# Performance work log

Measured on AMD Instinct MI355X. Metric: run time of the kernel, lower is better.

## Reference

```python
import jax, jax.numpy as jnp
import numpy as np

NEG_SLOPE = 0.2
LN_EPS = 1e-5


def _layer_norm(x, w, b):
    mu = jnp.mean(x, axis=-1, keepdims=True)
    var = jnp.mean((x - mu) ** 2, axis=-1, keepdims=True)
    return (x - mu) / jnp.sqrt(var + LN_EPS) * w + b


def setup_inputs() -> dict:
    N, E, R, H, D, HID, FF = 50000, 800000, 8, 4, 32, 128, 512
    key = jax.random.key(0)
    ks = jax.random.split(key, 12)
    s_w = float(np.sqrt(2.0 / (HID + HID)))  # xavier-ish scale
    return {
        "x": jax.random.normal(ks[0], (N, HID), jnp.float32),
        "weight": jax.random.normal(ks[1], (R, HID, HID), jnp.float32) * s_w,
        "root_weight": jax.random.normal(ks[2], (HID, HID), jnp.float32) * s_w,
        "edge_emb_table": jax.random.normal(ks[3], (R, HID), jnp.float32) * 0.01,
        "att_src": jax.random.normal(ks[4], (1, H, D), jnp.float32) * 0.1,
        "att_dst": jax.random.normal(ks[5], (1, H, D), jnp.float32) * 0.1,
        "att_edge": jax.random.normal(ks[6], (1, H, D), jnp.float32) * 0.1,
        "bias": jnp.zeros((HID,), jnp.float32),
        "norm1_w": jnp.ones((HID,), jnp.float32),
        "norm1_b": jnp.zeros((HID,), jnp.float32),
        "norm2_w": jnp.ones((HID,), jnp.float32),
        "norm2_b": jnp.zeros((HID,), jnp.float32),
        "ffn_w1": jax.random.normal(ks[7], (HID, FF), jnp.float32) * float(np.sqrt(2.0 / (HID + FF))),
        "ffn_b1": jnp.zeros((FF,), jnp.float32),
        "ffn_w2": jax.random.normal(ks[8], (FF, HID), jnp.float32) * float(np.sqrt(2.0 / (HID + FF))),
        "ffn_b2": jnp.zeros((HID,), jnp.float32),
        "edge_index": jax.random.randint(ks[9], (2, E), 0, N, jnp.int32),
        "edge_type": jax.random.randint(ks[10], (E,), 0, R, jnp.int32),
    }


def _rgat_conv(h, edge_index, edge_type, weight, root_weight, edge_emb_table,
               att_src, att_dst, att_edge, bias):
    N = h.shape[0]
    R = weight.shape[0]
    H, D = att_src.shape[1], att_src.shape[2]
    # relation-wise projection: [R, N, H, D]
    x_r = jnp.einsum('ni,rio->rno', h, weight).reshape(R, N, H, D)
    src, dst = edge_index[0], edge_index[1]
    x_src = x_r[edge_type, src]            # [E, H, D]
    x_dst = x_r[edge_type, dst]            # [E, H, D]
    edge_emb = edge_emb_table[edge_type].reshape(-1, H, D)
    alpha = (x_src * att_src).sum(-1) + (x_dst * att_dst).sum(-1) + (edge_emb * att_edge).sum(-1)  # [E, H]
    alpha = jax.nn.leaky_relu(alpha, NEG_SLOPE)
    # segment softmax over destination nodes
    amax = jax.ops.segment_max(alpha, dst, num_segments=N)  # [N, H]
    amax = jnp.where(jnp.isfinite(amax), amax, 0.0)
    ex = jnp.exp(alpha - amax[dst])
    den = jax.ops.segment_sum(ex, dst, num_segments=N)
    alpha = ex / (den[dst] + 1e-16)
    # dropout is identity in eval mode
    msg = x_src * alpha[..., None]         # [E, H, D]
    out = jax.ops.segment_sum(msg, dst, num_segments=N).reshape(N, H * D)
    return out + h @ root_weight + bias


def reference(x, weight, root_weight, edge_emb_table, att_src, att_dst, att_edge,
              bias, norm1_w, norm1_b, norm2_w, norm2_b,
              ffn_w1, ffn_b1, ffn_w2, ffn_b2, edge_index, edge_type):
    h = _layer_norm(x, norm1_w, norm1_b)
    h = _rgat_conv(h, edge_index, edge_type, weight, root_weight, edge_emb_table,
                   att_src, att_dst, att_edge, bias)
    h = jax.nn.elu(h)
    x = x + h
    h = _layer_norm(x, norm2_w, norm2_b)
    h = jax.nn.gelu(h @ ffn_w1 + ffn_b1, approximate=False) @ ffn_w2 + ffn_b2
    return x + h
```

## Files before the change

kernel.cpp:

```cpp
#include <hip/hip_runtime.h>
#include <hip/hip_bf16.h>
#include <math.h>

#define HID 128
#define NH  4
#define HD  32
#define FFD 512
#define RR  8
#define SCAN_B 1024
#define NB_SH 6

typedef __attribute__((ext_vector_type(8))) short bf16x8;
typedef __attribute__((ext_vector_type(4))) float f32x4;
typedef unsigned short u16;
typedef unsigned long long u64;

static __device__ __forceinline__ float bf2f(u16 u) {
    union { unsigned int i; float f; } v; v.i = ((unsigned int)u) << 16; return v.f;
}
static __device__ __forceinline__ u16 f2bf(float f) {
    union { float f; unsigned int i; } v; v.f = f;
    unsigned int x = v.i;
    return (u16)((x + 0x7fffu + ((x >> 16) & 1u)) >> 16);
}

__global__ void zeroout_kernel(float* out, int n) {
    int i = blockIdx.x * 256 + threadIdx.x;
    if (i < n) out[i] = 0.f;
}

__global__ void init_kernel(float* acc, int* deg2, int* bcnt, int NN, int NBK) {
    int i = blockIdx.x * 256 + threadIdx.x;
    if (i < NN * HID) acc[i] = 0.f;
    if (i < NN * RR) deg2[i] = 0;
    if (i < NBK * 16) bcnt[i] = 0;
}

__global__ void stats_kernel(const float* in, float* mu, float* rs, int NN) {
    int row = blockIdx.x * 4 + (threadIdx.x >> 6);
    int lane = threadIdx.x & 63;
    if (row >= NN) return;
    const float* p = in + (size_t)row * HID;
    float v0 = p[lane], v1 = p[lane + 64];
    float s = v0 + v1;
    #pragma unroll
    for (int o = 32; o > 0; o >>= 1) s += __shfl_xor(s, o, 64);
    float m = s * (1.0f / HID);
    float d0 = v0 - m, d1 = v1 - m;
    float q = d0 * d0 + d1 * d1;
    #pragma unroll
    for (int o = 32; o > 0; o >>= 1) q += __shfl_xor(q, o, 64);
    if (lane == 0) { mu[row] = m; rs[row] = rsqrtf(q * (1.0f / HID) + 1e-5f); }
}

__global__ void hnorm_kernel(const float* in, const float* mu, const float* rs,
                             const float* lw, const float* lb, u16* out, int NN) {
    int idx = blockIdx.x * 256 + threadIdx.x;
    if (idx >= NN * (HID / 8)) return;
    int row = idx >> 4;
    int k0 = (idx & 15) * 8;
    float m = mu[row], r = rs[row];
    const float* p = in + (size_t)row * HID + k0;
    float4 a0 = *(const float4*)p, a1 = *(const float4*)(p + 4);
    float4 w0 = *(const float4*)(lw + k0), w1 = *(const float4*)(lw + k0 + 4);
    float4 b0 = *(const float4*)(lb + k0), b1 = *(const float4*)(lb + k0 + 4);
    bf16x8 o;
    o[0] = (short)f2bf((a0.x - m) * r * w0.x + b0.x);
    o[1] = (short)f2bf((a0.y - m) * r * w0.y + b0.y);
    o[2] = (short)f2bf((a0.z - m) * r * w0.z + b0.z);
    o[3] = (short)f2bf((a0.w - m) * r * w0.w + b0.w);
    o[4] = (short)f2bf((a1.x - m) * r * w1.x + b1.x);
    o[5] = (short)f2bf((a1.y - m) * r * w1.y + b1.y);
    o[6] = (short)f2bf((a1.z - m) * r * w1.z + b1.z);
    o[7] = (short)f2bf((a1.w - m) * r * w1.w + b1.w);
    *(bf16x8*)(out + (size_t)row * HID + k0) = o;
}

__global__ void transpose_kernel(const float* w, const float* rootw,
                                 const float* w1, const float* w2,
                                 u16* WT, u16* rootT, u16* W1T, u16* W2T, int R) {
    int i = blockIdx.x * 256 + threadIdx.x;
    int nW = R * HID * HID;
    if (i < nW) {
        int r = i / (HID * HID); int rem = i % (HID * HID);
        int n = rem / HID, k = rem % HID;
        WT[i] = f2bf(w[r * HID * HID + k * HID + n]);
    } else if (i < nW + HID * HID) {
        int j = i - nW; int n = j / HID, k = j % HID;
        rootT[j] = f2bf(rootw[k * HID + n]);
    } else if (i < nW + HID * HID + FFD * HID) {
        int j = i - nW - HID * HID; int n = j / HID, k = j % HID;
        W1T[j] = f2bf(w1[k * FFD + n]);
    } else if (i < nW + HID * HID + FFD * HID + HID * FFD) {
        int j = i - nW - HID * HID - FFD * HID; int n = j / FFD, k = j % FFD;
        W2T[j] = f2bf(w2[k * HID + n]);
    }
}

__global__ void vsd_kernel(const float* w, const float* att_src, const float* att_dst,
                           u16* Vsd, int R) {
    int idx = blockIdx.x * 256 + threadIdx.x;
    if (idx >= 64 * HID) return;
    int np = idx >> 7, k = idx & 127;
    int isDst = np >> 5, rh = np & 31, r = rh >> 2, h = rh & 3;
    const float* av = (isDst ? att_dst : att_src) + h * HD;
    const float* wp = w + (size_t)r * HID * HID + (size_t)k * HID + h * HD;
    float s = 0.f;
    #pragma unroll
    for (int d = 0; d < HD; d++) s += wp[d] * av[d];
    Vsd[idx] = f2bf(s);
}

__global__ void ae_kernel(const float* emb, const float* att_edge, float* ae, int R) {
    int i = threadIdx.x;
    if (i >= R * NH) return;
    int r = i >> 2, h = i & 3;
    float s = 0.f;
    #pragma unroll
    for (int d = 0; d < HD; d++)
        s += emb[r * HID + h * HD + d] * att_edge[h * HD + d];
    ae[i] = s;
}

template <int EPI>
__global__ __launch_bounds__(256)
void gemmy_kernel(const u16* Araw, const u16* BT, u16* Cout, const float* bias,
                  int M, int N, int aOff, int cOff, int ytiles) {
    int w = threadIdx.x >> 6, lane = threadIdx.x & 63;
    int l15 = lane & 15, quad = lane >> 4;
    int m0 = blockIdx.x * 64 + w * 16;
    int rowA = m0 + l15; if (rowA > M - 1) rowA = M - 1;
    const u16* ap = Araw + (size_t)(aOff + rowA) * HID + quad * 8;
    bf16x8 a[4];
    #pragma unroll
    for (int kk = 0; kk < 4; kk++) a[kk] = *(const bf16x8*)(ap + kk * 32);

    __shared__ u16 tile[64][72];
    int rl2 = threadIdx.x >> 3, seg = threadIdx.x & 7;
    int ybase = blockIdx.y * ytiles;
    for (int yi = 0; yi < ytiles; yi++) {
        int n0 = (ybase + yi) * 64;
        f32x4 accr[4] = {};
        #pragma unroll
        for (int kk = 0; kk < 4; kk++) {
            #pragma unroll
            for (int t = 0; t < 4; t++) {
                const u16* bp = BT + (size_t)(n0 + t * 16 + l15) * HID + quad * 8 + kk * 32;
                bf16x8 bfrag = *(const bf16x8*)bp;
                accr[t] = __builtin_amdgcn_mfma_f32_16x16x32_bf16(a[kk], bfrag, accr[t], 0, 0, 0);
            }
        }
        if (yi > 0) __syncthreads();
        #pragma unroll
        for (int t = 0; t < 4; t++) {
            int col = n0 + t * 16 + l15;
            #pragma unroll
            for (int j = 0; j < 4; j++) {
                float v = accr[t][j];
                if constexpr (EPI == 2) {
                    v += bias[col];
                    v = 0.5f * v * (1.0f + erff(v * 0.70710678118654752f));
                }
                tile[w * 16 + quad * 4 + j][t * 16 + l15] = f2bf(v);
            }
        }
        __syncthreads();
        #pragma unroll
        for (int h = 0; h < 2; h++) {
            int rl = h * 32 + rl2;
            int row = blockIdx.x * 64 + rl;
            if (row < M) {
                u16* dst = Cout + (size_t)(cOff + row) * N + n0 + seg * 8;
                __builtin_nontemporal_store(*(const bf16x8*)&tile[rl][seg * 8],
                                            (bf16x8*)dst);
            }
        }
    }
}

template <int AM, int EPI>
__global__ __launch_bounds__(256)
void gemm_kernel(const void* Araw, const float* mu, const float* rs,
                 const float* lw, const float* lb,
                 const u16* BT, void* Cout, const float* bias,
                 const float* acc, const float* xin, const float* invden,
                 int M, int N, int K, int aOff, int cOff) {
    int w = threadIdx.x >> 6, lane = threadIdx.x & 63;
    int l15 = lane & 15, quad = lane >> 4;
    int m0 = blockIdx.x * 64 + w * 16;
    int n0 = blockIdx.y * 64;
    int rowA = m0 + l15; if (rowA > M - 1) rowA = M - 1;
    int gA = aOff + rowA;
    float muv = 0.f, rsv = 0.f;
    if (AM != 2) { muv = mu[gA]; rsv = rs[gA]; }

    f32x4 accr[4] = {};
    for (int kc = 0; kc < K; kc += 32) {
        bf16x8 a;
        if (AM == 0) {
            const float* ap = (const float*)Araw + (size_t)gA * K + quad * 8 + kc;
            float4 xa0 = *(const float4*)(ap);
            float4 xa1 = *(const float4*)(ap + 4);
            float4 w0 = *(const float4*)(lw + kc + quad * 8);
            float4 w1v = *(const float4*)(lw + kc + quad * 8 + 4);
            float4 b0 = *(const float4*)(lb + kc + quad * 8);
            float4 b1v = *(const float4*)(lb + kc + quad * 8 + 4);
            a[0] = (short)f2bf((xa0.x - muv) * rsv * w0.x + b0.x);
            a[1] = (short)f2bf((xa0.y - muv) * rsv * w0.y + b0.y);
            a[2] = (short)f2bf((xa0.z - muv) * rsv * w0.z + b0.z);
            a[3] = (short)f2bf((xa0.w - muv) * rsv * w0.w + b0.w);
            a[4] = (short)f2bf((xa1.x - muv) * rsv * w1v.x + b1v.x);
            a[5] = (short)f2bf((xa1.y - muv) * rsv * w1v.y + b1v.y);
            a[6] = (short)f2bf((xa1.z - muv) * rsv * w1v.z + b1v.z);
            a[7] = (short)f2bf((xa1.w - muv) * rsv * w1v.w + b1v.w);
        } else {
            const u16* ap = (const u16*)Araw + (size_t)gA * K + quad * 8 + kc;
            a = *(const bf16x8*)ap;
        }
        #pragma unroll
        for (int t = 0; t < 4; t++) {
            const u16* bp = BT + (size_t)(n0 + t * 16 + l15) * K + quad * 8 + kc;
            bf16x8 bfrag = *(const bf16x8*)bp;
            accr[t] = __builtin_amdgcn_mfma_f32_16x16x32_bf16(a, bfrag, accr[t], 0, 0, 0);
        }
    }

    if constexpr (EPI == 0 || EPI == 2) {
        __shared__ u16 tile[64][72];
        #pragma unroll
        for (int t = 0; t < 4; t++) {
            int col = n0 + t * 16 + l15;
            #pragma unroll
            for (int j = 0; j < 4; j++) {
                float v = accr[t][j];
                if (EPI == 2) {
                    v += bias[col];
                    v = 0.5f * v * (1.0f + erff(v * 0.70710678118654752f));
                }
                tile[w * 16 + quad * 4 + j][t * 16 + l15] = f2bf(v);
            }
        }
        __syncthreads();
        int rl2 = threadIdx.x >> 3, seg = threadIdx.x & 7;
        #pragma unroll
        for (int h = 0; h < 2; h++) {
            int rl = h * 32 + rl2;
            int row = blockIdx.x * 64 + rl;
            if (row < M) {
                u16* dst = (u16*)Cout + (size_t)(cOff + row) * N + n0 + seg * 8;
                __builtin_nontemporal_store(*(const bf16x8*)&tile[rl][seg * 8],
                                            (bf16x8*)dst);
            }
        }
    } else {
        #pragma unroll
        for (int t = 0; t < 4; t++) {
            int col = n0 + t * 16 + l15;
            #pragma unroll
            for (int j = 0; j < 4; j++) {
                int row = m0 + quad * 4 + j;
                if (row < M) {
                    float v = accr[t][j];
                    int grow = cOff + row;
                    size_t off = (size_t)grow * N + col;
                    if (EPI == 1) {
                        float msg = acc[(size_t)grow * HID + col]
                                  * invden[(size_t)grow * NH + (col >> 5)];
                        float o = v + msg + bias[col];
                        o = o > 0.f ? o : expm1f(o);
                        ((float*)Cout)[off] = xin[off] + o;
                    } else if (EPI == 3) {
                        ((float*)Cout)[off] = v + bias[col] + xin[off];
                    } else if (EPI == 5) {
                        float* tab = (float*)Cout;
                        if (col < 32) tab[(size_t)grow * 32 + col] = v;
                        else tab[(size_t)(M + grow) * 32 + (col - 32)] = v;
                    }
                }
            }
        }
    }
}

__global__ void deg_kernel(const int* ei, const int* et, int* deg2, int E, int NN) {
    int e = blockIdx.x * 256 + threadIdx.x;
    if (e >= E) return;
    int s = ei[e], d = ei[E + e], r = et[e];
    if ((unsigned)d < (unsigned)NN && (unsigned)r < (unsigned)RR &&
        (unsigned)s < (unsigned)NN)
        atomicAdd(&deg2[d * RR + r], 1);
}

__global__ void scan1_kernel(const int* in, int* out, int* bsum, int n) {
    __shared__ int buf[SCAN_B];
    int i = blockIdx.x * SCAN_B + threadIdx.x;
    int v = (i < n) ? in[i] : 0;
    buf[threadIdx.x] = v;
    __syncthreads();
    for (int s = 1; s < SCAN_B; s <<= 1) {
        int t = (threadIdx.x >= s) ? buf[threadIdx.x - s] : 0;
        __syncthreads();
        buf[threadIdx.x] += t;
        __syncthreads();
    }
    if (i < n) out[i] = buf[threadIdx.x] - v;
    if (threadIdx.x == SCAN_B - 1) bsum[blockIdx.x] = buf[SCAN_B - 1];
}

__global__ void scan2_kernel(int* bsum, int nb) {
    __shared__ int buf[SCAN_B];
    int v = (threadIdx.x < nb) ? bsum[threadIdx.x] : 0;
    buf[threadIdx.x] = v;
    __syncthreads();
    for (int s = 1; s < SCAN_B; s <<= 1) {
        int t = (threadIdx.x >= s) ? buf[threadIdx.x - s] : 0;
        __syncthreads();
        buf[threadIdx.x] += t;
        __syncthreads();
    }
    if (threadIdx.x < nb) bsum[threadIdx.x] = buf[threadIdx.x] - v;
    if (threadIdx.x == SCAN_B - 1) bsum[nb] = buf[SCAN_B - 1];
}

__global__ void scan3_kernel(int* out, int* curpos, const int* bsum, int n, int nb) {
    int i = blockIdx.x * SCAN_B + threadIdx.x;
    if (i < n) {
        int o = out[i] + bsum[blockIdx.x];
        out[i] = o; curpos[i] = o;
    }
    if (i == 0) out[n] = bsum[nb];
}

__global__ void fillA_kernel(const int* ei, const int* et, const int* offs2,
                             int* bcnt, u64* tmp, int E, int NN) {
    int e = blockIdx.x * 256 + threadIdx.x;
    if (e >= E) return;
    int s = ei[e], d = ei[E + e], r = et[e];
    if ((unsigned)d >= (unsigned)NN || (unsigned)r >= (unsigned)RR ||
        (unsigned)s >= (unsigned)NN) return;
    int b = d >> NB_SH;
    int base = offs2[(b << NB_SH) * RR];
    int pos = atomicAdd(&bcnt[b * 16], 1);
    tmp[base + pos] = ((u64)d << 32) | (unsigned)((r << 24) | s);
}

__global__ void fillB_kernel(const u64* tmp, const int* offs2,
                             int* curpos2, int* rs_arr, int NN) {
    int b = blockIdx.x;
    int n0 = b << NB_SH;
    int n1 = n0 + (1 << NB_SH); if (n1 > NN) n1 = NN;
    int base = offs2[n0 * RR];
    int end  = offs2[n1 * RR];
    for (int i = base + threadIdx.x; i < end; i += 256) {
        u64 t = tmp[i];
        int d = (int)(t >> 32);
        unsigned v = (unsigned)t;
        int r = v >> 24;
        int pos = atomicAdd(&curpos2[d * RR + r], 1);
        rs_arr[pos] = (int)v;
    }
}

__global__ void wgt_kernel(const int* offs2, const int* rs_arr,
                           const float* asad, const float* ae,
                           float* wgt, float* invden, int NN, int E) {
    int n = blockIdx.x * 4 + (threadIdx.x >> 6);
    if (n >= NN) return;
    int lane = threadIdx.x & 63;
    int el = lane >> 2, h = lane & 3;
    int p0 = offs2[n * RR], p1 = offs2[n * RR + RR];
    const float* ad = asad + (size_t)NN * 32;
    float base[RR];
    #pragma unroll
    for (int r = 0; r < RR; r++)
        base[r] = ad[(size_t)n * 32 + r * 4 + h] + ae[r * 4 + h];
    float mx = -1e30f;
    for (int p = p0 + el; p < p1; p += 16) {
        unsigned v = (unsigned)rs_arr[p];
        int r = v >> 24, s = v & 0xFFFFFF;
        float a = asad[(size_t)s * 32 + r * 4 + h] + base[r];
        a = a > 0.f ? a : 0.2f * a;
        wgt[(size_t)p * NH + h] = a;
        mx = fmaxf(mx, a);
    }
    #pragma unroll
    for (int o = 4; o < 64; o <<= 1) mx = fmaxf(mx, __shfl_xor(mx, o, 64));
    float den = 0.f;
    for (int p = p0 + el; p < p1; p += 16) {
        float ex = __expf(wgt[(size_t)p * NH + h] - mx);
        wgt[(size_t)p * NH + h] = ex;
        den += ex;
    }
    #pragma unroll
    for (int o = 4; o < 64; o <<= 1) den += __shfl_xor(den, o, 64);
    if (el == 0) invden[n * NH + h] = 1.0f / (den + 1e-16f);
}

__global__ void msg2_kernel(const int* offs2, const int* rs_arr, const float* wgt,
                            const u16* xp, float* acc, int rc, int nrel, int ldx,
                            int NN, int E, int single) {
    int n = blockIdx.x;
    int c = threadIdx.x, h = c >> 5;
    int p0 = offs2[n * RR + rc], p1 = offs2[n * RR + rc + nrel];
    float av;
    if (single) {
        av = 0.f;
    } else {
        if (p0 >= p1) return;
        av = acc[(size_t)n * HID + c];
    }
    for (int p = p0; p < p1; p++) {
        unsigned v = (unsigned)rs_arr[p];
        int r = (v >> 24) - rc;
        int s = v & 0xFFFFFF;
        av += wgt[(size_t)p * NH + h] * bf2f(xp[(size_t)s * ldx + r * HID + c]);
    }
    acc[(size_t)n * HID + c] = av;
}

extern "C" void kernel_launch(void* const* d_in, const int* in_sizes, int n_in,
                              void* d_out, int out_size, void* d_ws, size_t ws_size,
                              hipStream_t stream) {
    const float* x        = (const float*)d_in[0];
    const float* w        = (const float*)d_in[1];
    const float* rootw    = (const float*)d_in[2];
    const float* emb      = (const float*)d_in[3];
    const float* att_src  = (const float*)d_in[4];
    const float* att_dst  = (const float*)d_in[5];
    const float* att_edge = (const float*)d_in[6];
    const float* bias     = (const float*)d_in[7];
    const float* n1w      = (const float*)d_in[8];
    const float* n1b      = (const float*)d_in[9];
    const float* n2w      = (const float*)d_in[10];
    const float* n2b      = (const float*)d_in[11];
    const float* w1       = (const float*)d_in[12];
    const float* b1       = (const float*)d_in[13];
    const float* w2       = (const float*)d_in[14];
    const float* b2       = (const float*)d_in[15];
    const int* ei = (const int*)d_in[16];
    const int* et = (const int*)d_in[17];

    int NN = in_sizes[0] / HID;
    int R  = in_sizes[1] / (HID * HID);
    int E  = in_sizes[17];
    int NR = NN * RR;
    int NBK = (NN + (1 << NB_SH) - 1) >> NB_SH;

    char* p = (char*)d_ws;
    auto alloc = [&](size_t bytes) -> char* {
        char* q = p; p += (bytes + 255) & ~(size_t)255; return q;
    };
    int* offs2   = (int*)alloc((size_t)(NR + 1) * 4);
    int* rs_arr  = (int*)alloc((size_t)E * 4);
    u16* WTw   = (u16*)alloc((size_t)R * HID * HID * 2);
    u16* rootT = (u16*)alloc((size_t)HID * HID * 2);
    u16* W1T   = (u16*)alloc((size_t)FFD * HID * 2);
    u16* W2T   = (u16*)alloc((size_t)HID * FFD * 2);
    u16* Vsd   = (u16*)alloc((size_t)64 * HID * 2);
    float* ae  = (float*)alloc((size_t)R * NH * 4);
    float* mu1 = (float*)alloc((size_t)NN * 4);
    float* rs1 = (float*)alloc((size_t)NN * 4);
    float* mu2 = (float*)alloc((size_t)NN * 4);
    float* rs2 = (float*)alloc((size_t)NN * 4);
    float* asad   = (float*)alloc((size_t)NN * 64 * 4);
    float* invden = (float*)alloc((size_t)NN * NH * 4);
    float* wgt    = (float*)alloc((size_t)E * NH * 4);
    float* acc    = (float*)alloc((size_t)NN * HID * 4);

    int nbScan = (NR + SCAN_B - 1) / SCAN_B;
    int* deg2    = (int*)wgt;
    int* curpos2 = deg2 + NR;
    int* bsum    = curpos2 + NR;
    int* bcnt    = bsum + nbScan + 1;
    u64* tmp     = (u64*)(((size_t)(bcnt + NBK * 16) + 7) & ~(size_t)7);

    size_t usedFixed = (size_t)(p - (char*)d_ws);
    int nrel = 1;
    for (int t = 8; t > 1; t >>= 1) {
        if (ws_size >= usedFixed + (size_t)NN * HID * t * 2 + 256) { nrel = t; break; }
    }
    u16* xp = (u16*)alloc((size_t)NN * HID * nrel * 2);
    u16* u_ch = xp;
    u16* hbuf = (u16*)asad;
    float* x2 = (float*)d_out;

    size_t used = (size_t)(p - (char*)d_ws);
    if (used > ws_size) {
        zeroout_kernel<<<(out_size + 255) / 256, 256, 0, stream>>>((float*)d_out, out_size);
        return;
    }

    init_kernel<<<(NN * HID + 255) / 256, 256, 0, stream>>>(acc, deg2, bcnt, NN, NBK);
    stats_kernel<<<(NN + 3) / 4, 256, 0, stream>>>(x, mu1, rs1, NN);
    int nT = R * HID * HID + HID * HID + FFD * HID + HID * FFD;
    transpose_kernel<<<(nT + 255) / 256, 256, 0, stream>>>(w, rootw, w1, w2,
                                                           WTw, rootT, W1T, W2T, R);
    vsd_kernel<<<(64 * HID + 255) / 256, 256, 0, stream>>>(w, att_src, att_dst, Vsd, R);
    ae_kernel<<<1, 64, 0, stream>>>(emb, att_edge, ae, R);
    deg_kernel<<<(E + 255) / 256, 256, 0, stream>>>(ei, et, deg2, E, NN);
    scan1_kernel<<<nbScan, SCAN_B, 0, stream>>>(deg2, offs2, bsum, NR);
    scan2_kernel<<<1, SCAN_B, 0, stream>>>(bsum, nbScan);
    scan3_kernel<<<nbScan, SCAN_B, 0, stream>>>(offs2, curpos2, bsum, NR, nbScan);
    fillA_kernel<<<(E + 255) / 256, 256, 0, stream>>>(ei, et, offs2, bcnt, tmp, E, NN);
    fillB_kernel<<<NBK, 256, 0, stream>>>(tmp, offs2, curpos2, rs_arr, NN);

    int gxN = (NN + 63) / 64;
    gemm_kernel<0, 5><<<dim3(gxN, 1), 256, 0, stream>>>(
        x, mu1, rs1, n1w, n1b, Vsd, asad,
        nullptr, nullptr, nullptr, nullptr, NN, 64, HID, 0, 0);

    wgt_kernel<<<(NN + 3) / 4, 256, 0, stream>>>(
        offs2, rs_arr, asad, ae, wgt, invden, NN, E);

    hnorm_kernel<<<(NN * (HID / 8) + 255) / 256, 256, 0, stream>>>(
        x, mu1, rs1, n1w, n1b, hbuf, NN);

    if (nrel == RR) {
        gemmy_kernel<0><<<dim3(gxN, 2), 256, 0, stream>>>(
            hbuf, WTw, xp, nullptr, NN, HID * RR, 0, 0, 8);
        msg2_kernel<<<NN, HID, 0, stream>>>(offs2, rs_arr, wgt, xp, acc,
                                            0, RR, HID * RR, NN, E, 1);
    } else {
        for (int rc = 0; rc < RR; rc += nrel) {
            gemm_kernel<2, 0><<<dim3(gxN, (HID * nrel) / 64), 256, 0, stream>>>(
                hbuf, nullptr, nullptr, nullptr, nullptr, WTw + (size_t)rc * HID * HID,
                xp, nullptr, nullptr, nullptr, nullptr, NN, HID * nrel, HID, 0, 0);
            msg2_kernel<<<NN, HID, 0, stream>>>(offs2, rs_arr, wgt, xp, acc,
                                                rc, nrel, HID * nrel, NN, E, 0);
        }
    }

    gemm_kernel<2, 1><<<dim3(gxN, HID / 64), 256, 0, stream>>>(
        hbuf, nullptr, nullptr, nullptr, nullptr, rootT, x2, bias, acc, x, invden,
        NN, HID, HID, 0, 0);

    stats_kernel<<<(NN + 3) / 4, 256, 0, stream>>>(x2, mu2, rs2, NN);
    hnorm_kernel<<<(NN * (HID / 8) + 255) / 256, 256, 0, stream>>>(
        x2, mu2, rs2, n2w, n2b, hbuf, NN);
    int nchunk = (nrel >= 4) ? 1 : (nrel == 2 ? 2 : 4);
    int NCH = (NN + nchunk - 1) / nchunk;
    for (int j = 0; j < nchunk; j++) {
        int r0 = j * NCH;
        int Mc = NN - r0; if (Mc > NCH) Mc = NCH;
        if (Mc <= 0) continue;
        int gxc = (Mc + 63) / 64;
        gemmy_kernel<2><<<dim3(gxc, 2), 256, 0, stream>>>(
            hbuf, W1T, u_ch, b1, Mc, FFD, r0, 0, 4);
        gemm_kernel<2, 3><<<dim3(gxc, HID / 64), 256, 0, stream>>>(
            u_ch, nullptr, nullptr, nullptr, nullptr, W2T, (float*)d_out, b2,
            nullptr, x2, nullptr, Mc, HID, FFD, 0, r0);
    }
}
```

Before: 696.6 us.

## Aggregate normalized features per relation before projecting, fusing message pass with GEMM

Uses linearity to reorder the message pass. For each destination node and relation, the kernel first sums attention-weighted normalized input features, with one accumulator per head. It then multiplies those per-head sums by the relation weight with MFMA inside the same kernel. This removes the materialized N×8×128 bf16 projection buffer and its full write and gather traffic. It also drops zeroing of acc and the nontemporal stores. The cost is rounding the aggregated sums to bf16 and serial per-node edge loops inside 64-node blocks, which may load-imbalance.

```diff
diff --git a/kernel.cpp b/kernel.cpp
--- a/kernel.cpp
+++ b/kernel.cpp
@@ -29,9 +29,9 @@
     if (i < n) out[i] = 0.f;
 }
 
-__global__ void init_kernel(float* acc, int* deg2, int* bcnt, int NN, int NBK) {
+__global__ void init_kernel(float* acc, int* deg2, int* bcnt, int NN, int NBK, int zacc) {
     int i = blockIdx.x * 256 + threadIdx.x;
-    if (i < NN * HID) acc[i] = 0.f;
+    if (zacc && i < NN * HID) acc[i] = 0.f;
     if (i < NN * RR) deg2[i] = 0;
     if (i < NBK * 16) bcnt[i] = 0;
 }
@@ -171,8 +171,7 @@
             int row = blockIdx.x * 64 + rl;
             if (row < M) {
                 u16* dst = Cout + (size_t)(cOff + row) * N + n0 + seg * 8;
-                __builtin_nontemporal_store(*(const bf16x8*)&tile[rl][seg * 8],
-                                            (bf16x8*)dst);
+                *(bf16x8*)dst = *(const bf16x8*)&tile[rl][seg * 8];
             }
         }
     }
@@ -248,8 +247,7 @@
             int row = blockIdx.x * 64 + rl;
             if (row < M) {
                 u16* dst = (u16*)Cout + (size_t)(cOff + row) * N + n0 + seg * 8;
-                __builtin_nontemporal_store(*(const bf16x8*)&tile[rl][seg * 8],
-                                            (bf16x8*)dst);
+                *(bf16x8*)dst = *(const bf16x8*)&tile[rl][seg * 8];
             }
         }
     } else {
@@ -396,19 +394,86 @@
     if (el == 0) invden[n * NH + h] = 1.0f / (den + 1e-16f);
 }
 
+__global__ __launch_bounds__(512)
+void msgf_kernel(const int* offs2, const int* rs_arr, const float* wgt,
+                 const u16* hbuf, const u16* WTw, float* acc, int NN) {
+    __shared__ u16 S[4 * 64 * HID];
+    char* Sb = (char*)S;
+    int tid = threadIdx.x;
+    int wv = tid >> 6, lane = tid & 63;
+    int l15 = lane & 15, quad = lane >> 4;
+    int n0b = blockIdx.x << NB_SH;
+    int tm = wv & 3;
+    int cb = (wv >> 2) * 4;
+
+    f32x4 accr[4] = {};
+    for (int r = 0; r < RR; r++) {
+        #pragma unroll 1
+        for (int dd = 0; dd < 8; dd++) {
+            int d = wv * 8 + dd;
+            int n = n0b + d;
+            float a00 = 0.f, a01 = 0.f, a10 = 0.f, a11 = 0.f;
+            float a20 = 0.f, a21 = 0.f, a30 = 0.f, a31 = 0.f;
+            if (n < NN) {
+                int p0 = offs2[n * RR + r], p1 = offs2[n * RR + r + 1];
+                for (int p = p0; p < p1; p++) {
+                    unsigned v = (unsigned)rs_arr[p];
+                    unsigned z = *(const unsigned*)(hbuf
+                                    + (size_t)(v & 0xFFFFFFu) * HID + (lane << 1));
+                    float4 w4 = *(const float4*)(wgt + (size_t)p * NH);
+                    float x0 = bf2f((u16)z), x1 = bf2f((u16)(z >> 16));
+                    a00 += w4.x * x0; a01 += w4.x * x1;
+                    a10 += w4.y * x0; a11 += w4.y * x1;
+                    a20 += w4.z * x0; a21 += w4.z * x1;
+                    a30 += w4.w * x0; a31 += w4.w * x1;
+                }
+            }
+            int wb = (d << 8) + (lane << 2);
+            wb ^= (d & 7) << 4;
+            *(unsigned*)(Sb + wb)           = (unsigned)f2bf(a00) | ((unsigned)f2bf(a01) << 16);
+            *(unsigned*)(Sb + 16384 + wb)   = (unsigned)f2bf(a10) | ((unsigned)f2bf(a11) << 16);
+            *(unsigned*)(Sb + 32768 + wb)   = (unsigned)f2bf(a20) | ((unsigned)f2bf(a21) << 16);
+            *(unsigned*)(Sb + 49152 + wb)   = (unsigned)f2bf(a30) | ((unsigned)f2bf(a31) << 16);
+        }
+        __syncthreads();
+        const u16* Wr = WTw + (size_t)r * HID * HID;
+        int arow = tm * 16 + l15;
+        #pragma unroll
+        for (int ks = 0; ks < 4; ks++) {
+            #pragma unroll
+            for (int ct = 0; ct < 4; ct++) {
+                int ctt = cb + ct;
+                int hh = ctt >> 1;
+                int rb = (hh << 14) + (arow << 8) + (ks << 6) + (quad << 4);
+                rb ^= (arow & 7) << 4;
+                bf16x8 afrag = *(const bf16x8*)(Sb + rb);
+                const u16* bp = Wr + (size_t)(ctt * 16 + l15) * HID + ks * 32 + quad * 8;
+                bf16x8 bfrag = *(const bf16x8*)bp;
+                accr[ct] = __builtin_amdgcn_mfma_f32_16x16x32_bf16(afrag, bfrag, accr[ct], 0, 0, 0);
+            }
+        }
+        __syncthreads();
+    }
+    #pragma unroll
+    for (int ct = 0; ct < 4; ct++) {
+        int col = (cb + ct) * 16 + l15;
+        #pragma unroll
+        for (int j = 0; j < 4; j++) {
+            int row = tm * 16 + quad * 4 + j;
+            int n = n0b + row;
+            if (n < NN) acc[(size_t)n * HID + col] = accr[ct][j];
+        }
+    }
+}
+
 __global__ void msg2_kernel(const int* offs2, const int* rs_arr, const float* wgt,
                             const u16* xp, float* acc, int rc, int nrel, int ldx,
-                            int NN, int E, int single) {
+                            int NN, int E) {
     int n = blockIdx.x;
     int c = threadIdx.x, h = c >> 5;
     int p0 = offs2[n * RR + rc], p1 = offs2[n * RR + rc + nrel];
-    float av;
-    if (single) {
-        av = 0.f;
-    } else {
-        if (p0 >= p1) return;
-        av = acc[(size_t)n * HID + c];
-    }
+    if (p0 >= p1) return;
+    float av = acc[(size_t)n * HID + c];
     for (int p = p0; p < p1; p++) {
         unsigned v = (unsigned)rs_arr[p];
         int r = (v >> 24) - rc;
@@ -490,7 +555,10 @@
         return;
     }
 
-    init_kernel<<<(NN * HID + 255) / 256, 256, 0, stream>>>(acc, deg2, bcnt, NN, NBK);
+    int single = (nrel == RR) ? 1 : 0;
+    int initN = single ? (NR > NBK * 16 ? NR : NBK * 16) : NN * HID;
+    init_kernel<<<(initN + 255) / 256, 256, 0, stream>>>(acc, deg2, bcnt, NN, NBK,
+                                                         single ? 0 : 1);
     stats_kernel<<<(NN + 3) / 4, 256, 0, stream>>>(x, mu1, rs1, NN);
     int nT = R * HID * HID + HID * HID + FFD * HID + HID * FFD;
     transpose_kernel<<<(nT + 255) / 256, 256, 0, stream>>>(w, rootw, w1, w2,
@@ -515,18 +583,15 @@
     hnorm_kernel<<<(NN * (HID / 8) + 255) / 256, 256, 0, stream>>>(
         x, mu1, rs1, n1w, n1b, hbuf, NN);
 
-    if (nrel == RR) {
-        gemmy_kernel<0><<<dim3(gxN, 2), 256, 0, stream>>>(
-            hbuf, WTw, xp, nullptr, NN, HID * RR, 0, 0, 8);
-        msg2_kernel<<<NN, HID, 0, stream>>>(offs2, rs_arr, wgt, xp, acc,
-                                            0, RR, HID * RR, NN, E, 1);
+    if (single) {
+        msgf_kernel<<<NBK, 512, 0, stream>>>(offs2, rs_arr, wgt, hbuf, WTw, acc, NN);
     } else {
         for (int rc = 0; rc < RR; rc += nrel) {
             gemm_kernel<2, 0><<<dim3(gxN, (HID * nrel) / 64), 256, 0, stream>>>(
                 hbuf, nullptr, nullptr, nullptr, nullptr, WTw + (size_t)rc * HID * HID,
                 xp, nullptr, nullptr, nullptr, nullptr, NN, HID * nrel, HID, 0, 0);
             msg2_kernel<<<NN, HID, 0, stream>>>(offs2, rs_arr, wgt, xp, acc,
-                                                rc, nrel, HID * nrel, NN, E, 0);
+                                                rc, nrel, HID * nrel, NN, E);
         }
     }
 
```

New measurement: 800.8 us. 1.15x slower.
